# Optimization experiments

Measured on AMD Instinct MI355X. Metric: run time of the kernel, lower is better.

## Reference

```python
import jax, jax.numpy as jnp
import numpy as np

# hardcoded constants from the source module
C = 768      # n_embd
H = 8        # n_head
HS = C // H  # head_size = 96
E = 8        # n_experts
K = 2        # top_k
L = 12       # n_layer
V = 95       # vocab_size = len(chars)
BS = 64      # block_size
B, T = 16, 64


def setup_inputs() -> dict:
    key = jax.random.key(0)
    ks = iter(jax.random.split(key, 32))
    nrm = lambda shape: jax.random.normal(next(ks), shape, dtype=jnp.float32) * 0.02
    d = {
        'idx': jax.random.randint(next(ks), (B, T), 0, V),
        'tok_emb': nrm((V, C)),
        'pos_emb': nrm((BS, C)),
        # attention (per-layer stacked); per-head q/k/v linears concatenated into [C, C]
        'Wq': nrm((L, C, C)), 'Wk': nrm((L, C, C)), 'Wv': nrm((L, C, C)),
        'Wo': nrm((L, C, C)), 'bo': jnp.zeros((L, C), jnp.float32),
        # MoE
        'gate_W': nrm((L, C, E)), 'gate_b': jnp.zeros((L, E), jnp.float32),
        'W1': nrm((L, E, C, 4 * C)), 'b1': jnp.zeros((L, E, 4 * C), jnp.float32),
        'W2': nrm((L, E, 4 * C, C)), 'b2': jnp.zeros((L, E, C), jnp.float32),
        # layernorms
        'ln1_g': jnp.ones((L, C), jnp.float32), 'ln1_b': jnp.zeros((L, C), jnp.float32),
        'ln2_g': jnp.ones((L, C), jnp.float32), 'ln2_b': jnp.zeros((L, C), jnp.float32),
        'lnf_g': jnp.ones((C,), jnp.float32), 'lnf_b': jnp.zeros((C,), jnp.float32),
        # lm head
        'head_W': nrm((C, V)), 'head_b': jnp.zeros((V,), jnp.float32),
    }
    return d


def _layernorm(x, g, b, eps=1e-5):
    mu = x.mean(-1, keepdims=True)
    var = ((x - mu) ** 2).mean(-1, keepdims=True)
    return (x - mu) * jax.lax.rsqrt(var + eps) * g + b


def _moe(x, gw, gb, w1, b1, w2, b2):
    # x: [B,T,C]; compute all experts densely then combine top-k (faithful to source)
    xf = x.reshape(-1, C)                                  # [N,C]
    probs = jax.nn.softmax(xf @ gw + gb, axis=-1)          # [N,E]
    tp, ti = jax.lax.top_k(probs, K)                       # [N,K]
    tp = tp / tp.sum(-1, keepdims=True)
    h = jax.nn.gelu(jnp.einsum('nc,ech->neh', xf, w1) + b1, approximate=False)
    eo = jnp.einsum('neh,ehc->nec', h, w2) + b2            # [N,E,C]
    sel = jnp.take_along_axis(eo, ti[:, :, None], axis=1)  # [N,K,C]
    return (tp[:, :, None] * sel).sum(1).reshape(x.shape)


def _forward(idx, tok_emb, pos_emb, Wq, Wk, Wv, Wo, bo, gate_W, gate_b, W1, b1,
             W2, b2, ln1_g, ln1_b, ln2_g, ln2_b, lnf_g, lnf_b, head_W, head_b):
    Bc, Tc = idx.shape
    x = tok_emb[idx] + pos_emb[jnp.arange(Tc) % BS]        # [B,T,C]
    mask = jnp.tril(jnp.ones((Tc, Tc), bool))

    def block(x, p):
        q = (x @ p['Wq']).reshape(Bc, Tc, H, HS)
        k = (x @ p['Wk']).reshape(Bc, Tc, H, HS)
        v = (x @ p['Wv']).reshape(Bc, Tc, H, HS)
        att = jnp.einsum('bqhd,bkhd->bhqk', q, k) * (HS ** -0.5)
        att = jnp.where(mask, att, -jnp.inf)
        w = jax.nn.softmax(att, axis=-1)
        o = jnp.einsum('bhqk,bkhd->bqhd', w, v).reshape(Bc, Tc, C)
        y = o @ p['Wo'] + p['bo']
        x = _layernorm(x + y, p['g1'], p['b1n'])
        y = _moe(x, p['gw'], p['gb'], p['w1'], p['bb1'], p['w2'], p['bb2'])
        x = _layernorm(x + y, p['g2'], p['b2n'])
        return x, None

    params = {'Wq': Wq, 'Wk': Wk, 'Wv': Wv, 'Wo': Wo, 'bo': bo,
              'gw': gate_W, 'gb': gate_b, 'w1': W1, 'bb1': b1, 'w2': W2, 'bb2': b2,
              'g1': ln1_g, 'b1n': ln1_b, 'g2': ln2_g, 'b2n': ln2_b}
    x, _ = jax.lax.scan(block, x, params)
    x = _layernorm(x, lnf_g, lnf_b)
    return x @ head_W + head_b                              # [B,T,V]


def reference(idx, tok_emb, pos_emb, Wq, Wk, Wv, Wo, bo, gate_W, gate_b, W1, b1,
              W2, b2, ln1_g, ln1_b, ln2_g, ln2_b, lnf_g, lnf_b, head_W, head_b):
    return _forward(idx, tok_emb, pos_emb, Wq, Wk, Wv, Wo, bo, gate_W, gate_b,
                    W1, b1, W2, b2, ln1_g, ln1_b, ln2_g, ln2_b, lnf_g, lnf_b,
                    head_W, head_b)
```

## Files before the change

kernel.cpp:

```cpp
#include <hip/hip_runtime.h>
#include <math.h>

#define C    768
#define HN   8
#define HS   96
#define NE   8
#define NL   12
#define NV   95
#define TT   64
#define NB   16
#define NTOK 1024
#define H4   3072
#define NKR  2048
#define NKRP 2176
#define MC   (NTOK * C)

typedef __attribute__((ext_vector_type(8))) short short8;
typedef __attribute__((ext_vector_type(4))) float floatx4;

union U16x8 { uint4 u; short8 s; };
static __device__ __forceinline__ short8 as_s8(uint4 u) { U16x8 x; x.u = u; return x.s; }
static __device__ __forceinline__ uint4 ror16x4(uint4 q) {
  uint4 r;
  r.x = (q.x >> 16) | (q.x << 16);
  r.y = (q.y >> 16) | (q.y << 16);
  r.z = (q.z >> 16) | (q.z << 16);
  r.w = (q.w >> 16) | (q.w << 16);
  return r;
}

static __device__ __forceinline__ unsigned pack_split(float f) {
  unsigned u = __float_as_uint(f);
  unsigned h = (u + 0x7fffu + ((u >> 16) & 1u)) >> 16;
  float d = f - __uint_as_float(h << 16);
  unsigned v = __float_as_uint(d);
  unsigned l = (v + 0x7fffu + ((v >> 16) & 1u)) >> 16;
  return h | (l << 16);
}
static __device__ __forceinline__ float unpack_split(unsigned w) {
  return __uint_as_float(w << 16) + __uint_as_float(w & 0xffff0000u);
}

template<int OUTMODE>
static __device__ __forceinline__ void gemm_body(
    const unsigned* __restrict__ Ap, const int* __restrict__ perm,
    const float* __restrict__ W, const float* __restrict__ bias,
    float* __restrict__ outF, unsigned* __restrict__ outP,
    int row0, int Mend, int col0, int N, int K, int kbeg, int kend)
{
  __shared__ __align__(16) unsigned Bt[2][128 * 32];
  const int tid  = threadIdx.x;
  const int lane = tid & 63, wv = tid >> 6;
  const int l16  = lane & 15, lq = lane >> 4;
  const int sw   = (l16 & 7) << 2;

  int ra0 = row0 + wv * 32 + l16;
  int ra1 = ra0 + 16;
  if (perm) { ra0 = perm[ra0]; ra1 = perm[ra1]; }
  const unsigned* A0 = Ap + (size_t)ra0 * K;
  const unsigned* A1 = Ap + (size_t)ra1 * K;

  const int bcol = tid & 127;
  const int bqh  = (tid >> 7) * 4;
  int bcg = col0 + bcol; if (bcg >= N) bcg = N - 1;
  const float* Wb = W + bcg;
  const int bswz = (bcol & 7) << 2;
  float bw[16];
  auto loadB = [&](int kpos) {
    #pragma unroll
    for (int qq = 0; qq < 4; ++qq) {
      int kr = kpos + (bqh + qq) * 4;
      #pragma unroll
      for (int i = 0; i < 4; ++i) bw[qq * 4 + i] = Wb[(size_t)(kr + i) * N];
    }
  };
  auto writeB = [&](int buf) {
    #pragma unroll
    for (int qq = 0; qq < 4; ++qq) {
      uint4 u;
      u.x = pack_split(bw[qq * 4 + 0]); u.y = pack_split(bw[qq * 4 + 1]);
      u.z = pack_split(bw[qq * 4 + 2]); u.w = pack_split(bw[qq * 4 + 3]);
      *(uint4*)&Bt[buf][bcol * 32 + (((bqh + qq) * 4) ^ bswz)] = u;
    }
  };

  uint4 ac0[2], ac1[2];
  auto loadA = [&](int kpos, uint4* d0, uint4* d1) {
    const unsigned* p = A0 + kpos;
    d0[0] = *(const uint4*)(p + lq * 4);
    d0[1] = *(const uint4*)(p + 16 + lq * 4);
    p = A1 + kpos;
    d1[0] = *(const uint4*)(p + lq * 4);
    d1[1] = *(const uint4*)(p + 16 + lq * 4);
  };

  floatx4 acc[2][8];
  #pragma unroll
  for (int h = 0; h < 2; ++h)
    #pragma unroll
    for (int f = 0; f < 8; ++f) acc[h][f] = (floatx4){0, 0, 0, 0};

  const int ns = (kend - kbeg) >> 5;
  loadB(kbeg); loadA(kbeg, ac0, ac1); writeB(0);

  for (int s = 0; s < ns; ++s) {
    const int b = s & 1;
    __syncthreads();
    const int kn = kbeg + ((s + 1 < ns) ? (s + 1) * 32 : s * 32);
    loadB(kn);
    uint4 na0[2], na1[2];
    loadA(kn, na0, na1);
    const unsigned* bp = Bt[b];
    #pragma unroll
    for (int f = 0; f < 8; ++f) {
      const unsigned* base = bp + (f * 16 + l16) * 32;
      uint4 q0 = *(const uint4*)(base + ((4 * lq) ^ sw));
      uint4 q1 = *(const uint4*)(base + ((16 + 4 * lq) ^ sw));
      short8 b0 = as_s8(q0), b0r = as_s8(ror16x4(q0));
      short8 b1 = as_s8(q1), b1r = as_s8(ror16x4(q1));
      short8 a00 = as_s8(ac0[0]), a01 = as_s8(ac0[1]);
      short8 a10 = as_s8(ac1[0]), a11 = as_s8(ac1[1]);
      acc[0][f] = __builtin_amdgcn_mfma_f32_16x16x32_bf16(a00, b0,  acc[0][f], 0, 0, 0);
      acc[1][f] = __builtin_amdgcn_mfma_f32_16x16x32_bf16(a10, b0,  acc[1][f], 0, 0, 0);
      acc[0][f] = __builtin_amdgcn_mfma_f32_16x16x32_bf16(a00, b0r, acc[0][f], 0, 0, 0);
      acc[1][f] = __builtin_amdgcn_mfma_f32_16x16x32_bf16(a10, b0r, acc[1][f], 0, 0, 0);
      acc[0][f] = __builtin_amdgcn_mfma_f32_16x16x32_bf16(a01, b1,  acc[0][f], 0, 0, 0);
      acc[1][f] = __builtin_amdgcn_mfma_f32_16x16x32_bf16(a11, b1,  acc[1][f], 0, 0, 0);
      acc[0][f] = __builtin_amdgcn_mfma_f32_16x16x32_bf16(a01, b1r, acc[0][f], 0, 0, 0);
      acc[1][f] = __builtin_amdgcn_mfma_f32_16x16x32_bf16(a11, b1r, acc[1][f], 0, 0, 0);
    }
    if (s + 1 < ns) writeB(b ^ 1);
    ac0[0] = na0[0]; ac0[1] = na0[1]; ac1[0] = na1[0]; ac1[1] = na1[1];
  }

  const int rb = row0 + wv * 32 + lq * 4;
  #pragma unroll
  for (int h = 0; h < 2; ++h) {
    #pragma unroll
    for (int f = 0; f < 8; ++f) {
      int cc = col0 + f * 16 + l16;
      if (cc < N) {
        float bb = (OUTMODE == 1) ? bias[cc] : 0.f;
        #pragma unroll
        for (int r = 0; r < 4; ++r) {
          int rr = rb + h * 16 + r;
          if (rr < Mend) {
            float v = acc[h][f][r] + bb;
            if (OUTMODE == 1) {
              v = 0.5f * v * (1.f + erff(v * 0.70710678118654752f));
              outP[(size_t)rr * N + cc] = pack_split(v);
            } else {
              outF[(size_t)rr * N + cc] = v;
            }
          }
        }
      }
    }
  }
}

static __device__ __forceinline__ void expert_range(const int* counts, int e,
                                                    int& off, int& cnt) {
  off = 0; cnt = 0;
  #pragma unroll
  for (int i = 0; i < NE; ++i) {
    int c = counts[i];
    if (i < e) off += c;
    if (i == e) cnt = c;
  }
}

__global__ void __launch_bounds__(256) k_qkv(const unsigned* xp, const float* Wq,
    const float* Wk, const float* Wv, float* qkvp) {
  int z = blockIdx.z, mat = z >> 1, ch = z & 1;
  const float* W = mat == 0 ? Wq : (mat == 1 ? Wk : Wv);
  gemm_body<2>(xp, nullptr, W, nullptr, qkvp + (size_t)z * MC, nullptr,
               blockIdx.y * 128, NTOK, blockIdx.x * 128, C, C, ch * 384, (ch + 1) * 384);
}

__global__ void __launch_bounds__(256) k_wo(const unsigned* op, const float* W,
    float* wop) {
  int ch = blockIdx.z;
  gemm_body<2>(op, nullptr, W, nullptr, wop + (size_t)ch * MC, nullptr,
               blockIdx.y * 128, NTOK, blockIdx.x * 128, C, C, ch * 128, (ch + 1) * 128);
}

__global__ void __launch_bounds__(256) k_w1(const unsigned* xp, const int* perm,
    const float* W1, const float* b1, unsigned* Hgp, const int* counts) {
  int e = blockIdx.z, off, cnt;
  expert_range(counts, e, off, cnt);
  int r0 = blockIdx.y * 128;
  if (r0 >= cnt) return;
  gemm_body<1>(xp, perm, W1 + (size_t)e * C * H4, b1 + (size_t)e * H4, nullptr, Hgp,
               off + r0, off + cnt, blockIdx.x * 128, H4, C, 0, C);
}

__global__ void __launch_bounds__(256) k_w2(const unsigned* Hgp, const float* W2,
    float* Ypart, const int* counts) {
  int z = blockIdx.z, e = z >> 2, ch = z & 3;
  int off, cnt;
  expert_range(counts, e, off, cnt);
  int r0 = blockIdx.y * 128;
  if (r0 >= cnt) return;
  gemm_body<2>(Hgp, nullptr, W2 + (size_t)e * H4 * C, nullptr,
               Ypart + (size_t)ch * NKRP * C, nullptr,
               off + r0, off + cnt, blockIdx.x * 128, C, H4, ch * 768, (ch + 1) * 768);
}

__global__ void __launch_bounds__(256) k_head(const unsigned* xp, const float* W,
    float* hpart) {
  int ch = blockIdx.z;
  gemm_body<2>(xp, nullptr, W, nullptr, hpart + (size_t)ch * NTOK * NV, nullptr,
               blockIdx.y * 128, NTOK, 0, NV, C, ch * 64, (ch + 1) * 64);
}

__global__ void k_headsum(const float* hpart, const float* headb, float* out) {
  int n = blockIdx.x, c = threadIdx.x;
  if (c < NV) {
    size_t i = (size_t)n * NV + c;
    float s = headb[c];
    #pragma unroll
    for (int ch = 0; ch < 12; ++ch) s += hpart[i + (size_t)ch * NTOK * NV];
    out[i] = s;
  }
}

__global__ void k_embed(const int* __restrict__ idx, const float* __restrict__ tok,
                        const float* __restrict__ pos, unsigned* __restrict__ xp) {
  int n = blockIdx.x; int t = n & (TT - 1);
  int token = idx[n];
  for (int j = threadIdx.x; j < C; j += 256)
    xp[(size_t)n * C + j] = pack_split(tok[(size_t)token * C + j] + pos[(size_t)t * C + j]);
}

static __device__ __forceinline__ void ln_finish(int tid, float* v, const float* g,
                                                 const float* bb, unsigned* outrow,
                                                 float* sp) {
  int lane = tid & 63, wid = tid >> 6;
  float s = v[0] + v[1] + v[2];
  for (int o = 32; o; o >>= 1) s += __shfl_down(s, o);
  if (!lane) sp[wid] = s;
  __syncthreads();
  float mean = (sp[0] + sp[1] + sp[2] + sp[3]) * (1.f / C);
  __syncthreads();
  float d0 = v[0] - mean, d1 = v[1] - mean, d2 = v[2] - mean;
  float qq = d0 * d0 + d1 * d1 + d2 * d2;
  for (int o = 32; o; o >>= 1) qq += __shfl_down(qq, o);
  if (!lane) sp[wid] = qq;
  __syncthreads();
  float var = (sp[0] + sp[1] + sp[2] + sp[3]) * (1.f / C);
  float rs = rsqrtf(var + 1e-5f);
  #pragma unroll
  for (int i = 0; i < 3; ++i) {
    int c = tid + i * 256;
    v[i] = (v[i] - mean) * rs * g[c] + bb[c];
    outrow[c] = pack_split(v[i]);
  }
}

__global__ void __launch_bounds__(256) k_ln1g(unsigned* __restrict__ xp,
    const float* __restrict__ wop, const float* __restrict__ bo,
    const float* __restrict__ g, const float* __restrict__ bb,
    const float* __restrict__ gW, const float* __restrict__ gb,
    int* __restrict__ ti, float* __restrict__ tp, int* __restrict__ pos,
    int* __restrict__ counts) {
  int n = blockIdx.x; int tid = threadIdx.x;
  __shared__ float sp[4];
  __shared__ float gs[4][NE];
  float v[3];
  #pragma unroll
  for (int i = 0; i < 3; ++i) {
    int c = tid + i * 256;
    size_t gi = (size_t)n * C + c;
    float acc = unpack_split(xp[gi]) + bo[c];
    #pragma unroll
    for (int ch = 0; ch < 6; ++ch) acc += wop[gi + (size_t)ch * MC];
    v[i] = acc;
  }
  ln_finish(tid, v, g, bb, xp + (size_t)n * C, sp);
  float a[NE];
  #pragma unroll
  for (int e = 0; e < NE; ++e) a[e] = 0.f;
  #pragma unroll
  for (int i = 0; i < 3; ++i) {
    int c = tid + i * 256;
    const float* gr = gW + (size_t)c * NE;
    #pragma unroll
    for (int e = 0; e < NE; ++e) a[e] += v[i] * gr[e];
  }
  int lane = tid & 63, wid = tid >> 6;
  #pragma unroll
  for (int e = 0; e < NE; ++e)
    for (int o = 32; o; o >>= 1) a[e] += __shfl_down(a[e], o);
  if (!lane)
    #pragma unroll
    for (int e = 0; e < NE; ++e) gs[wid][e] = a[e];
  __syncthreads();
  if (tid == 0) {
    float p[NE]; float m = -1e30f;
    #pragma unroll
    for (int e = 0; e < NE; ++e) {
      p[e] = gs[0][e] + gs[1][e] + gs[2][e] + gs[3][e] + gb[e];
      m = fmaxf(m, p[e]);
    }
    float den = 0.f;
    #pragma unroll
    for (int e = 0; e < NE; ++e) { p[e] = expf(p[e] - m); den += p[e]; }
    float inv = 1.f / den;
    #pragma unroll
    for (int e = 0; e < NE; ++e) p[e] *= inv;
    int e0 = 0;
    for (int e = 1; e < NE; ++e) if (p[e] > p[e0]) e0 = e;
    int e1 = -1;
    for (int e = 0; e < NE; ++e) if (e != e0 && (e1 < 0 || p[e] > p[e1])) e1 = e;
    float ss = p[e0] + p[e1];
    int p0 = atomicAdd(&counts[e0], 1), p1 = atomicAdd(&counts[e1], 1);
    ti[n * 2] = e0;  ti[n * 2 + 1] = e1;
    pos[n * 2] = p0; pos[n * 2 + 1] = p1;
    tp[n * 2] = p[e0] / ss; tp[n * 2 + 1] = p[e1] / ss;
  }
}

__global__ void k_perm(const int* __restrict__ ti, const int* __restrict__ pos,
                       const int* __restrict__ counts, int* __restrict__ rowOf,
                       int* __restrict__ perm) {
  int a = blockIdx.x * 256 + threadIdx.x;
  if (a >= NKRP) return;
  if (a >= NKR) { perm[a] = 0; return; }
  int e = ti[a];
  int off = 0;
  #pragma unroll
  for (int i = 0; i < NE; ++i) if (i < e) off += counts[i];
  int row = off + pos[a];
  rowOf[a] = row;
  perm[row] = a >> 1;
}

__global__ void __launch_bounds__(256) k_ln_moe(unsigned* __restrict__ xp,
    const float* __restrict__ Ypart, const int* __restrict__ rowOf,
    const int* __restrict__ ti, const float* __restrict__ tp,
    const float* __restrict__ b2, const float* __restrict__ g,
    const float* __restrict__ bb) {
  int n = blockIdx.x; int tid = threadIdx.x;
  __shared__ float sp[4];
  int r0 = rowOf[n * 2], r1 = rowOf[n * 2 + 1];
  int e0 = ti[n * 2], e1 = ti[n * 2 + 1];
  float w0 = tp[n * 2], w1 = tp[n * 2 + 1];
  const float* bz0 = b2 + (size_t)e0 * C;
  const float* bz1 = b2 + (size_t)e1 * C;
  float v[3];
  #pragma unroll
  for (int i = 0; i < 3; ++i) {
    int c = tid + i * 256;
    float y0 = bz0[c], y1 = bz1[c];
    #pragma unroll
    for (int ch = 0; ch < 4; ++ch) {
      const float* pl = Ypart + (size_t)ch * NKRP * C;
      y0 += pl[(size_t)r0 * C + c];
      y1 += pl[(size_t)r1 * C + c];
    }
    v[i] = unpack_split(xp[(size_t)n * C + c]) + w0 * y0 + w1 * y1;
  }
  ln_finish(tid, v, g, bb, xp + (size_t)n * C, sp);
}

__global__ void __launch_bounds__(256) k_lnf(unsigned* __restrict__ xp,
    const float* __restrict__ g, const float* __restrict__ bb) {
  int n = blockIdx.x; int tid = threadIdx.x;
  __shared__ float sp[4];
  float v[3];
  #pragma unroll
  for (int i = 0; i < 3; ++i) v[i] = unpack_split(xp[(size_t)n * C + tid + i * 256]);
  ln_finish(tid, v, g, bb, xp + (size_t)n * C, sp);
}

__global__ void __launch_bounds__(256) k_attn(const float* __restrict__ qkvp,
    unsigned* __restrict__ op, int* __restrict__ counts) {
  int bh = blockIdx.x; int b = bh >> 3, h = bh & 7;
  int tid = threadIdx.x;
  if (bh == 0 && tid < NE) counts[tid] = 0;
  __shared__ float qs[TT][HS];
  __shared__ float kv[TT][HS];
  const float* q0 = qkvp;                  const float* q1 = qkvp + MC;
  const float* k0 = qkvp + 2 * (size_t)MC; const float* k1 = qkvp + 3 * (size_t)MC;
  const float* v0 = qkvp + 4 * (size_t)MC; const float* v1 = qkvp + 5 * (size_t)MC;
  for (int i = tid; i < TT * HS; i += 256) {
    int t = i / HS, d = i % HS;
    size_t gi = (size_t)(b * TT + t) * C + h * HS + d;
    qs[t][d] = q0[gi] + q1[gi];
    kv[t][d] = k0[gi] + k1[gi];
  }
  __syncthreads();
  int r = tid >> 2, g = tid & 3;
  const float scale = 0.10206207261596575f;
  float sreg[16];
  {
    const floatx4* q4 = (const floatx4*)&qs[r][0];
    #pragma unroll
    for (int j = 0; j < 16; ++j) {
      int kk = g * 16 + j;
      float s = -1e30f;
      if (kk <= r) {
        const floatx4* k4 = (const floatx4*)&kv[kk][0];
        float a2 = 0.f;
        #pragma unroll
        for (int d4 = 0; d4 < HS / 4; ++d4) {
          floatx4 a = q4[d4], bbv = k4[d4];
          a2 += a[0]*bbv[0] + a[1]*bbv[1] + a[2]*bbv[2] + a[3]*bbv[3];
        }
        s = a2 * scale;
      }
      sreg[j] = s;
    }
  }
  float m = sreg[0];
  #pragma unroll
  for (int j = 1; j < 16; ++j) m = fmaxf(m, sreg[j]);
  m = fmaxf(m, __shfl_xor(m, 1));
  m = fmaxf(m, __shfl_xor(m, 2));
  float den = 0.f;
  #pragma unroll
  for (int j = 0; j < 16; ++j) { sreg[j] = expf(sreg[j] - m); den += sreg[j]; }
  den += __shfl_xor(den, 1);
  den += __shfl_xor(den, 2);
  float inv = 1.f / den;
  __syncthreads();
  float (*psc)[TT] = (float(*)[TT])&qs[0][0];
  #pragma unroll
  for (int j = 0; j < 16; ++j) psc[r][g * 16 + j] = sreg[j] * inv;
  for (int i = tid; i < TT * HS; i += 256) {
    int t = i / HS, d = i % HS;
    size_t gi = (size_t)(b * TT + t) * C + h * HS + d;
    kv[t][d] = v0[gi] + v1[gi];
  }
  __syncthreads();
  floatx4 accv[6];
  #pragma unroll
  for (int cc = 0; cc < 6; ++cc) accv[cc] = (floatx4){0, 0, 0, 0};
  for (int kk = 0; kk < TT; ++kk) {
    float wgt = psc[r][kk];
    const floatx4* v4 = (const floatx4*)&kv[kk][0];
    #pragma unroll
    for (int cc = 0; cc < 6; ++cc) accv[cc] += wgt * v4[g * 6 + cc];
  }
  unsigned* orow = op + (size_t)(b * TT + r) * C + h * HS + g * 24;
  #pragma unroll
  for (int cc = 0; cc < 6; ++cc)
    #pragma unroll
    for (int mm = 0; mm < 4; ++mm) orow[cc * 4 + mm] = pack_split(accv[cc][mm]);
}

extern "C" void kernel_launch(void* const* d_in, const int* in_sizes, int n_in,
                              void* d_out, int out_size, void* d_ws, size_t ws_size,
                              hipStream_t stream) {
  const int*   idx   = (const int*)d_in[0];
  const float* tok   = (const float*)d_in[1];
  const float* pose  = (const float*)d_in[2];
  const float* Wq    = (const float*)d_in[3];
  const float* Wk    = (const float*)d_in[4];
  const float* Wv    = (const float*)d_in[5];
  const float* Wo    = (const float*)d_in[6];
  const float* bo    = (const float*)d_in[7];
  const float* gW    = (const float*)d_in[8];
  const float* gb    = (const float*)d_in[9];
  const float* W1    = (const float*)d_in[10];
  const float* b1    = (const float*)d_in[11];
  const float* W2    = (const float*)d_in[12];
  const float* b2    = (const float*)d_in[13];
  const float* ln1g  = (const float*)d_in[14];
  const float* ln1b  = (const float*)d_in[15];
  const float* ln2g  = (const float*)d_in[16];
  const float* ln2b  = (const float*)d_in[17];
  const float* lnfg  = (const float*)d_in[18];
  const float* lnfb  = (const float*)d_in[19];
  const float* headW = (const float*)d_in[20];
  const float* headb = (const float*)d_in[21];
  float* out = (float*)d_out;

  if (ws_size < (size_t)160 * 1024 * 1024) return;
  char* w = (char*)d_ws;
  auto allocU = [&](size_t n) { unsigned* p = (unsigned*)w; w += n * 4; return p; };
  auto allocF = [&](size_t n) { float* p = (float*)w; w += n * 4; return p; };
  unsigned* xp    = allocU((size_t)MC);
  unsigned* op    = allocU((size_t)MC);
  float*    qkvp  = allocF((size_t)6 * MC);
  float*    wop   = allocF((size_t)6 * MC);
  unsigned* Hgp   = allocU((size_t)NKRP * H4);
  float*    Ypart = allocF((size_t)4 * NKRP * C);
  float*    hpart = allocF((size_t)12 * NTOK * NV);
  float*    tp    = allocF(NKR);
  int* ti     = (int*)w; w += NKR * 4;
  int* posA   = (int*)w; w += NKR * 4;
  int* rowOf  = (int*)w; w += NKR * 4;
  int* perm   = (int*)w; w += NKRP * 4;
  int* counts = (int*)w; w += NE * 4;

  k_embed<<<NTOK, 256, 0, stream>>>(idx, tok, pose, xp);

  for (int l = 0; l < NL; ++l) {
    k_qkv<<<dim3(6, 8, 6), 256, 0, stream>>>(
        xp, Wq + (size_t)l * C * C, Wk + (size_t)l * C * C, Wv + (size_t)l * C * C, qkvp);
    k_attn<<<NB * HN, 256, 0, stream>>>(qkvp, op, counts);
    k_wo<<<dim3(6, 8, 6), 256, 0, stream>>>(op, Wo + (size_t)l * C * C, wop);
    k_ln1g<<<NTOK, 256, 0, stream>>>(xp, wop, bo + (size_t)l * C,
        ln1g + (size_t)l * C, ln1b + (size_t)l * C,
        gW + (size_t)l * C * NE, gb + (size_t)l * NE, ti, tp, posA, counts);
    k_perm<<<(NKRP + 255) / 256, 256, 0, stream>>>(ti, posA, counts, rowOf, perm);
    k_w1<<<dim3(24, 8, 8), 256, 0, stream>>>(xp, perm,
        W1 + (size_t)l * NE * C * H4, b1 + (size_t)l * NE * H4, Hgp, counts);
    k_w2<<<dim3(6, 8, 32), 256, 0, stream>>>(Hgp,
        W2 + (size_t)l * NE * H4 * C, Ypart, counts);
    k_ln_moe<<<NTOK, 256, 0, stream>>>(xp, Ypart, rowOf, ti, tp,
        b2 + (size_t)l * NE * C, ln2g + (size_t)l * C, ln2b + (size_t)l * C);
  }

  k_lnf<<<NTOK, 256, 0, stream>>>(xp, lnfg, lnfb);
  k_head<<<dim3(1, 8, 12), 256, 0, stream>>>(xp, headW, hpart);
  k_headsum<<<NTOK, 128, 0, stream>>>(hpart, headb, out);
}
```

Measured before the change: 4.120 ms.

## Pre-pack weights into tiled split-bf16 layout and stage B tiles via direct-to-LDS loads

A new prep kernel runs on every call before the layers. It converts all fp32 weight matrices into a swizzled, tile-contiguous hi/lo bf16 packed layout in workspace. The GEMM body then fills its B tiles with global_load_lds 16-byte direct-to-LDS loads. This replaces the per-block fp32 loads, split conversion and LDS stores, which were repeated by every row tile. The cost is an extra full read and write of about 1.8 GB of weights per call, and the workspace requirement rises to 2.2 GB. If the workspace is smaller than that, the function returns early. A clamp on A row indices is also added.

```diff
diff --git a/kernel.cpp b/kernel.cpp
--- a/kernel.cpp
+++ b/kernel.cpp
@@ -41,10 +41,42 @@
   return __uint_as_float(w << 16) + __uint_as_float(w & 0xffff0000u);
 }
 
+static __device__ __forceinline__ void gload_lds16(const unsigned* g, unsigned* l) {
+  __builtin_amdgcn_global_load_lds(
+      (const __attribute__((address_space(1))) unsigned*)g,
+      (__attribute__((address_space(3))) unsigned*)l, 16, 0, 0);
+}
+
+__global__ void __launch_bounds__(256) k_prep(const float* __restrict__ src,
+    unsigned* __restrict__ dst, int K, int N, long matStride, long dstMatStride) {
+  int nt = blockIdx.x, kt = blockIdx.y, mz = blockIdx.z;
+  const float* W = src + (size_t)mz * matStride;
+  unsigned* out = dst + (size_t)mz * dstMatStride
+                + ((size_t)nt * (K >> 5) + kt) * 4096;
+  __shared__ float ls[32 * 130];
+  int tid = threadIdx.x;
+  int n0 = nt * 128, k0 = kt * 32;
+  #pragma unroll
+  for (int p = 0; p < 16; ++p) {
+    int idx = p * 256 + tid;
+    int k = idx >> 7, c = idx & 127;
+    int n = n0 + c;
+    ls[k * 130 + c] = (n < N) ? W[(size_t)(k0 + k) * N + n] : 0.f;
+  }
+  __syncthreads();
+  #pragma unroll
+  for (int p = 0; p < 16; ++p) {
+    int idx = p * 256 + tid;
+    int col = idx >> 5, ks = idx & 31;
+    int k = ks ^ ((col & 7) << 2);
+    out[idx] = pack_split(ls[k * 130 + col]);
+  }
+}
+
 template<int OUTMODE>
 static __device__ __forceinline__ void gemm_body(
     const unsigned* __restrict__ Ap, const int* __restrict__ perm,
-    const float* __restrict__ W, const float* __restrict__ bias,
+    const unsigned* __restrict__ Wt, const float* __restrict__ bias,
     float* __restrict__ outF, unsigned* __restrict__ outP,
     int row0, int Mend, int col0, int N, int K, int kbeg, int kend)
 {
@@ -56,32 +88,19 @@
 
   int ra0 = row0 + wv * 32 + l16;
   int ra1 = ra0 + 16;
+  if (ra0 > Mend - 1) ra0 = Mend - 1;
+  if (ra1 > Mend - 1) ra1 = Mend - 1;
   if (perm) { ra0 = perm[ra0]; ra1 = perm[ra1]; }
   const unsigned* A0 = Ap + (size_t)ra0 * K;
   const unsigned* A1 = Ap + (size_t)ra1 * K;
 
-  const int bcol = tid & 127;
-  const int bqh  = (tid >> 7) * 4;
-  int bcg = col0 + bcol; if (bcg >= N) bcg = N - 1;
-  const float* Wb = W + bcg;
-  const int bswz = (bcol & 7) << 2;
-  float bw[16];
-  auto loadB = [&](int kpos) {
-    #pragma unroll
-    for (int qq = 0; qq < 4; ++qq) {
-      int kr = kpos + (bqh + qq) * 4;
-      #pragma unroll
-      for (int i = 0; i < 4; ++i) bw[qq * 4 + i] = Wb[(size_t)(kr + i) * N];
-    }
-  };
-  auto writeB = [&](int buf) {
-    #pragma unroll
-    for (int qq = 0; qq < 4; ++qq) {
-      uint4 u;
-      u.x = pack_split(bw[qq * 4 + 0]); u.y = pack_split(bw[qq * 4 + 1]);
-      u.z = pack_split(bw[qq * 4 + 2]); u.w = pack_split(bw[qq * 4 + 3]);
-      *(uint4*)&Bt[buf][bcol * 32 + (((bqh + qq) * 4) ^ bswz)] = u;
-    }
+  const unsigned* tsrc = Wt + ((size_t)(col0 >> 7) * (K >> 5) + (kbeg >> 5)) * 4096;
+  auto stageB = [&](int buf, int kt) {
+    const unsigned* s = tsrc + (size_t)kt * 4096 + wv * 1024 + lane * 4;
+    unsigned* d = &Bt[buf][wv * 1024];
+    #pragma unroll
+    for (int j = 0; j < 4; ++j)
+      gload_lds16(s + j * 256, d + j * 256);
   };
 
   uint4 ac0[2], ac1[2];
@@ -101,13 +120,14 @@
     for (int f = 0; f < 8; ++f) acc[h][f] = (floatx4){0, 0, 0, 0};
 
   const int ns = (kend - kbeg) >> 5;
-  loadB(kbeg); loadA(kbeg, ac0, ac1); writeB(0);
+  stageB(0, 0);
+  loadA(kbeg, ac0, ac1);
 
   for (int s = 0; s < ns; ++s) {
     const int b = s & 1;
     __syncthreads();
+    if (s + 1 < ns) stageB(b ^ 1, s + 1);
     const int kn = kbeg + ((s + 1 < ns) ? (s + 1) * 32 : s * 32);
-    loadB(kn);
     uint4 na0[2], na1[2];
     loadA(kn, na0, na1);
     const unsigned* bp = Bt[b];
@@ -129,7 +149,6 @@
       acc[0][f] = __builtin_amdgcn_mfma_f32_16x16x32_bf16(a01, b1r, acc[0][f], 0, 0, 0);
       acc[1][f] = __builtin_amdgcn_mfma_f32_16x16x32_bf16(a11, b1r, acc[1][f], 0, 0, 0);
     }
-    if (s + 1 < ns) writeB(b ^ 1);
     ac0[0] = na0[0]; ac0[1] = na0[1]; ac1[0] = na1[0]; ac1[1] = na1[1];
   }
 
@@ -170,15 +189,15 @@
   }
 }
 
-__global__ void __launch_bounds__(256) k_qkv(const unsigned* xp, const float* Wq,
-    const float* Wk, const float* Wv, float* qkvp) {
+__global__ void __launch_bounds__(256) k_qkv(const unsigned* xp, const unsigned* Wq,
+    const unsigned* Wk, const unsigned* Wv, float* qkvp) {
   int z = blockIdx.z, mat = z >> 1, ch = z & 1;
-  const float* W = mat == 0 ? Wq : (mat == 1 ? Wk : Wv);
+  const unsigned* W = mat == 0 ? Wq : (mat == 1 ? Wk : Wv);
   gemm_body<2>(xp, nullptr, W, nullptr, qkvp + (size_t)z * MC, nullptr,
                blockIdx.y * 128, NTOK, blockIdx.x * 128, C, C, ch * 384, (ch + 1) * 384);
 }
 
-__global__ void __launch_bounds__(256) k_wo(const unsigned* op, const float* W,
+__global__ void __launch_bounds__(256) k_wo(const unsigned* op, const unsigned* W,
     float* wop) {
   int ch = blockIdx.z;
   gemm_body<2>(op, nullptr, W, nullptr, wop + (size_t)ch * MC, nullptr,
@@ -186,7 +205,7 @@
 }
 
 __global__ void __launch_bounds__(256) k_w1(const unsigned* xp, const int* perm,
-    const float* W1, const float* b1, unsigned* Hgp, const int* counts) {
+    const unsigned* W1, const float* b1, unsigned* Hgp, const int* counts) {
   int e = blockIdx.z, off, cnt;
   expert_range(counts, e, off, cnt);
   int r0 = blockIdx.y * 128;
@@ -195,7 +214,7 @@
                off + r0, off + cnt, blockIdx.x * 128, H4, C, 0, C);
 }
 
-__global__ void __launch_bounds__(256) k_w2(const unsigned* Hgp, const float* W2,
+__global__ void __launch_bounds__(256) k_w2(const unsigned* Hgp, const unsigned* W2,
     float* Ypart, const int* counts) {
   int z = blockIdx.z, e = z >> 2, ch = z & 3;
   int off, cnt;
@@ -207,7 +226,7 @@
                off + r0, off + cnt, blockIdx.x * 128, C, H4, ch * 768, (ch + 1) * 768);
 }
 
-__global__ void __launch_bounds__(256) k_head(const unsigned* xp, const float* W,
+__global__ void __launch_bounds__(256) k_head(const unsigned* xp, const unsigned* W,
     float* hpart) {
   int ch = blockIdx.z;
   gemm_body<2>(xp, nullptr, W, nullptr, hpart + (size_t)ch * NTOK * NV, nullptr,
@@ -477,10 +496,17 @@
   const float* headb = (const float*)d_in[21];
   float* out = (float*)d_out;
 
-  if (ws_size < (size_t)160 * 1024 * 1024) return;
+  if (ws_size < (size_t)2200 * 1024 * 1024) return;
   char* w = (char*)d_ws;
   auto allocU = [&](size_t n) { unsigned* p = (unsigned*)w; w += n * 4; return p; };
   auto allocF = [&](size_t n) { float* p = (float*)w; w += n * 4; return p; };
+  unsigned* Wqp = allocU((size_t)NL * C * C);
+  unsigned* Wkp = allocU((size_t)NL * C * C);
+  unsigned* Wvp = allocU((size_t)NL * C * C);
+  unsigned* Wop = allocU((size_t)NL * C * C);
+  unsigned* W1p = allocU((size_t)NL * NE * C * H4);
+  unsigned* W2p = allocU((size_t)NL * NE * H4 * C);
+  unsigned* Whp = allocU((size_t)24 * 4096);
   unsigned* xp    = allocU((size_t)MC);
   unsigned* op    = allocU((size_t)MC);
   float*    qkvp  = allocF((size_t)6 * MC);
@@ -495,26 +521,34 @@
   int* perm   = (int*)w; w += NKRP * 4;
   int* counts = (int*)w; w += NE * 4;
 
+  k_prep<<<dim3(6, 24, 12), 256, 0, stream>>>(Wq, Wqp, C, C, (long)C * C, (long)C * C);
+  k_prep<<<dim3(6, 24, 12), 256, 0, stream>>>(Wk, Wkp, C, C, (long)C * C, (long)C * C);
+  k_prep<<<dim3(6, 24, 12), 256, 0, stream>>>(Wv, Wvp, C, C, (long)C * C, (long)C * C);
+  k_prep<<<dim3(6, 24, 12), 256, 0, stream>>>(Wo, Wop, C, C, (long)C * C, (long)C * C);
+  k_prep<<<dim3(24, 24, 96), 256, 0, stream>>>(W1, W1p, C, H4, (long)C * H4, (long)C * H4);
+  k_prep<<<dim3(6, 96, 96), 256, 0, stream>>>(W2, W2p, H4, C, (long)H4 * C, (long)H4 * C);
+  k_prep<<<dim3(1, 24, 1), 256, 0, stream>>>(headW, Whp, C, NV, 0, 0);
+
   k_embed<<<NTOK, 256, 0, stream>>>(idx, tok, pose, xp);
 
   for (int l = 0; l < NL; ++l) {
     k_qkv<<<dim3(6, 8, 6), 256, 0, stream>>>(
-        xp, Wq + (size_t)l * C * C, Wk + (size_t)l * C * C, Wv + (size_t)l * C * C, qkvp);
+        xp, Wqp + (size_t)l * C * C, Wkp + (size_t)l * C * C, Wvp + (size_t)l * C * C, qkvp);
     k_attn<<<NB * HN, 256, 0, stream>>>(qkvp, op, counts);
-    k_wo<<<dim3(6, 8, 6), 256, 0, stream>>>(op, Wo + (size_t)l * C * C, wop);
+    k_wo<<<dim3(6, 8, 6), 256, 0, stream>>>(op, Wop + (size_t)l * C * C, wop);
     k_ln1g<<<NTOK, 256, 0, stream>>>(xp, wop, bo + (size_t)l * C,
         ln1g + (size_t)l * C, ln1b + (size_t)l * C,
         gW + (size_t)l * C * NE, gb + (size_t)l * NE, ti, tp, posA, counts);
     k_perm<<<(NKRP + 255) / 256, 256, 0, stream>>>(ti, posA, counts, rowOf, perm);
     k_w1<<<dim3(24, 8, 8), 256, 0, stream>>>(xp, perm,
-        W1 + (size_t)l * NE * C * H4, b1 + (size_t)l * NE * H4, Hgp, counts);
+        W1p + (size_t)l * NE * C * H4, b1 + (size_t)l * NE * H4, Hgp, counts);
     k_w2<<<dim3(6, 8, 32), 256, 0, stream>>>(Hgp,
-        W2 + (size_t)l * NE * H4 * C, Ypart, counts);
+        W2p + (size_t)l * NE * H4 * C, Ypart, counts);
     k_ln_moe<<<NTOK, 256, 0, stream>>>(xp, Ypart, rowOf, ti, tp,
         b2 + (size_t)l * NE * C, ln2g + (size_t)l * C, ln2b + (size_t)l * C);
   }
 
   k_lnf<<<NTOK, 256, 0, stream>>>(xp, lnfg, lnfb);
-  k_head<<<dim3(1, 8, 12), 256, 0, stream>>>(xp, headW, hpart);
+  k_head<<<dim3(1, 8, 12), 256, 0, stream>>>(xp, Whp, hpart);
   k_headsum<<<NTOK, 128, 0, stream>>>(hpart, headb, out);
 }
```

After: 4.090 ms. Within noise of the previous version (-0.7%).
